# Optimization experiments

Hardware: AMD Instinct MI355X
Metric: run time of the kernel (lower is better)

The kernel has to match this reference:

```python
import jax, jax.numpy as jnp
import numpy as np

IN_C, OUT_C, K = 256, 256, 3

def setup_inputs() -> dict:
    key = jax.random.key(0)
    kx, kw, kb = jax.random.split(key, 3)
    x = jax.random.normal(kx, (32, IN_C, 56, 56), dtype=jnp.float32)
    # kaiming-like scale for conv weight
    fan_in = IN_C * K * K
    weight = jax.random.normal(kw, (OUT_C, IN_C, K, K), dtype=jnp.float32) / np.sqrt(fan_in)
    bias = jax.random.normal(kb, (OUT_C,), dtype=jnp.float32) * 0.01
    return {"x": x, "weight": weight, "bias": bias}

def reference(x, weight, bias):
    # SparseConv2d computes an (approximately lossless, threshold=1e-6)
    # block-sparse conv2d; exact math == dense conv2d, stride 1, pad 1.
    y = jax.lax.conv_general_dilated(
        x, weight,
        window_strides=(1, 1),
        padding=((1, 1), (1, 1)),
        dimension_numbers=("NCHW", "OIHW", "NCHW"),
    )
    return y + bias[None, :, None, None]
```

## Files before the change

kernel.cpp:

```cpp
#include <hip/hip_runtime.h>
#include <hip/hip_bf16.h>

#define IN_C  256
#define OUT_C 256
#define HH 56
#define WW 56
#define NN 32
#define XT_H 58
#define XT_W 64
#define WT_BYTES (8*9*256*32*2)

#define XS_BYTES 24576
#define LDS_TOTAL (2*XS_BYTES)

using short8 = __attribute__((ext_vector_type(8))) short;
using f32x4  = __attribute__((ext_vector_type(4))) float;

__device__ __forceinline__ void gload_lds16(const void* g, void* l) {
  __builtin_amdgcn_global_load_lds((const __attribute__((address_space(1))) void*)g,
                                   (__attribute__((address_space(3))) void*)l,
                                   16, 0, 0);
}

#define VMWAIT(N) asm volatile("s_waitcnt vmcnt(" #N ")" ::: "memory")

__global__ void k_prep(const float* __restrict__ x, const float* __restrict__ w,
                       __hip_bfloat16* __restrict__ wt, __hip_bfloat16* __restrict__ xt) {
  const int b = blockIdx.x, tid = threadIdx.x;

  if (b >= NN * XT_H) {
    const int base = (b - NN * XT_H) * 1024;
#pragma unroll
    for (int k = 0; k < 4; ++k) {
      int idx = base + k * 256 + tid;
      int kw = idx % 3; int t1 = idx / 3;
      int kh = t1 % 3;  int t2 = t1 / 3;
      int ic = t2 % IN_C; int oc = t2 / IN_C;
      int tap = kh * 3 + kw;
      wt[((((ic >> 5) * 9 + tap) * 256 + oc) * 32) + (ic & 31)] = __float2bfloat16(w[idx]);
    }
    return;
  }

  const int n = b / XT_H, hp = b % XT_H;
  __hip_bfloat16* row = xt + (size_t)(n * XT_H + hp) * XT_W * 256;

  if (hp == 0 || hp == XT_H - 1) {
    int4 z; z.x = z.y = z.z = z.w = 0;
#pragma unroll
    for (int k = 0; k < 8; ++k) ((int4*)row)[k * 256 + tid] = z;
    return;
  }

  const int h = hp - 1;
  __shared__ __hip_bfloat16 tile[56][264];

  {
    const int ic = tid;
    const float* src = x + (((size_t)n * IN_C + ic) * HH + h) * WW;
#pragma unroll
    for (int j = 0; j < 14; ++j) {
      float4 v = ((const float4*)src)[j];
      tile[4 * j + 0][ic] = __float2bfloat16(v.x);
      tile[4 * j + 1][ic] = __float2bfloat16(v.y);
      tile[4 * j + 2][ic] = __float2bfloat16(v.z);
      tile[4 * j + 3][ic] = __float2bfloat16(v.w);
    }
  }
  {
    int4 z; z.x = z.y = z.z = z.w = 0;
    int cell = tid >> 5, s = tid & 31;
    int wp = (cell == 0) ? 0 : (56 + cell);
    ((int4*)(row + (size_t)wp * 256))[s] = z;
  }
  __syncthreads();
#pragma unroll
  for (int k = 0; k < 7; ++k) {
    int e = k * 256 + tid;
    int wq = e >> 5, seg = e & 31;
    short8 v = *(const short8*)&tile[wq][seg * 8];
    *(short8*)(row + (size_t)(wq + 1) * 256 + seg * 8) = v;
  }
}

__global__ __launch_bounds__(256, 3) void k_conv(
    const __hip_bfloat16* __restrict__ wt, const __hip_bfloat16* __restrict__ xt,
    const float* __restrict__ bias, float* __restrict__ out) {
  extern __shared__ __align__(16) char lds[];
  char* xs_c = lds;

  const int tid  = threadIdx.x;
  const int wid  = tid >> 6, lane = tid & 63;
  const int cc   = lane & 15, g = lane >> 4;
  const int wn   = wid & 1,  wm = wid >> 1;

  const int work = (blockIdx.x & 7) * 224 + (blockIdx.x >> 3);
  const int n   = work / 56;
  const int rem = work - n * 56;
  const int q   = rem >> 2, oh = rem & 3;
  const int h0  = q * 4;

  int xoff[7];
#pragma unroll
  for (int pt = 0; pt < 7; ++pt) {
    int p = wm * 112 + pt * 16 + cc;
    int rp = p / 56, wp = p - rp * 56;
    xoff[pt] = rp * 4096 + wp * 64 + g * 16;
  }
  const int ocb = oh * 64 + wn * 32;
  const __hip_bfloat16* wlane = wt + (size_t)(ocb + cc) * 32 + g * 8;

  f32x4 acc[2][7];
#pragma unroll
  for (int a = 0; a < 2; ++a)
#pragma unroll
    for (int bb = 0; bb < 7; ++bb) acc[a][bb] = (f32x4){0.f, 0.f, 0.f, 0.f};

  const __hip_bfloat16* xtn = xt + (size_t)(n * XT_H + h0) * XT_W * 256;

  auto stage_x = [&](int buf, int ch) {
#pragma unroll
    for (int i = 0; i < 6; ++i) {
      int s = wid * 6 + i;
      int rowc = s >> 2, colq = s & 3;
      const __hip_bfloat16* src = xtn + (size_t)(rowc * 64 + colq * 16 + (lane >> 2)) * 256
                                      + ch * 32 + (lane & 3) * 8;
      gload_lds16(src, xs_c + buf * XS_BYTES + rowc * 4096 + colq * 1024);
    }
  };
  auto loadw1 = [&](int ph, int oct) -> short8 {
    return *(const short8*)(wlane + (size_t)ph * 8192 + oct * 512);
  };

  short8 wA, wB, wC;

  stage_x(0, 0);
  __builtin_amdgcn_sched_barrier(0);
  wA = loadw1(0, 0);
  wB = loadw1(0, 1);

#define MFMA7(W_, oct_) do {                                                          \
    __builtin_amdgcn_s_setprio(1);                                                    \
    _Pragma("unroll")                                                                 \
    for (int pt = 0; pt < 7; ++pt)                                                    \
      acc[oct_][pt] = __builtin_amdgcn_mfma_f32_16x16x32_bf16(W_, xf[pt], acc[oct_][pt], 0, 0, 0); \
    __builtin_amdgcn_s_setprio(0);                                                    \
  } while (0)

#define PHASE(ph_, kh_, kw_, T0_, T1_, T2_) do {                                      \
    short8 xf[7];                                                                     \
    _Pragma("unroll")                                                                 \
    for (int pt = 0; pt < 7; ++pt)                                                    \
      xf[pt] = *(const short8*)(xb + xoff[pt] + (kh_) * 4096 + (kw_) * 64);           \
    T2_ = loadw1((ph_) + 1, 0);                                                       \
    MFMA7(T0_, 0);                                                                    \
    T0_ = loadw1((ph_) + 1, 1);                                                       \
    MFMA7(T1_, 1);                                                                    \
  } while (0)

  for (int ch = 0; ch < 8; ++ch) {
    VMWAIT(2);
    __builtin_amdgcn_s_barrier();
    if (ch < 7) {
      stage_x((ch + 1) & 1, ch + 1);
      __builtin_amdgcn_sched_barrier(0);
    }
    const char* xb = xs_c + ((ch & 1) ? XS_BYTES : 0);
    const int ph0 = ch * 9;
    PHASE(ph0 + 0, 0, 0, wA, wB, wC);
    PHASE(ph0 + 1, 0, 1, wC, wA, wB);
    PHASE(ph0 + 2, 0, 2, wB, wC, wA);
    PHASE(ph0 + 3, 1, 0, wA, wB, wC);
    PHASE(ph0 + 4, 1, 1, wC, wA, wB);
    PHASE(ph0 + 5, 1, 2, wB, wC, wA);
    PHASE(ph0 + 6, 2, 0, wA, wB, wC);
    PHASE(ph0 + 7, 2, 1, wC, wA, wB);
    PHASE(ph0 + 8, 2, 2, wB, wC, wA);
  }
#undef PHASE
#undef MFMA7

  int rp_[7], wp_[7];
#pragma unroll
  for (int pt = 0; pt < 7; ++pt) {
    int p = wm * 112 + pt * 16 + cc;
    rp_[pt] = p / 56; wp_[pt] = p - rp_[pt] * 56;
  }
#pragma unroll
  for (int oct = 0; oct < 2; ++oct) {
    const int oc0 = ocb + oct * 16 + 4 * g;
#pragma unroll
    for (int r = 0; r < 4; ++r) {
      const float bv = bias[oc0 + r];
      const size_t obase = ((size_t)n * OUT_C + (oc0 + r)) * (HH * WW);
#pragma unroll
      for (int pt = 0; pt < 7; ++pt)
        out[obase + (size_t)(h0 + rp_[pt]) * 56 + wp_[pt]] = acc[oct][pt][r] + bv;
    }
  }
}

extern "C" void kernel_launch(void* const* d_in, const int* in_sizes, int n_in,
                              void* d_out, int out_size, void* d_ws, size_t ws_size,
                              hipStream_t stream) {
  const float* x    = (const float*)d_in[0];
  const float* w    = (const float*)d_in[1];
  const float* bias = (const float*)d_in[2];
  float* out        = (float*)d_out;

  __hip_bfloat16* wt = (__hip_bfloat16*)d_ws;
  __hip_bfloat16* xt = (__hip_bfloat16*)((char*)d_ws + WT_BYTES);

  hipFuncSetAttribute((const void*)k_conv,
                      hipFuncAttributeMaxDynamicSharedMemorySize, LDS_TOTAL);

  k_prep<<<NN * XT_H + 576, 256, 0, stream>>>(x, w, wt, xt);
  k_conv<<<NN * 14 * 4, 256, LDS_TOTAL, stream>>>(wt, xt, bias, out);
}
```

Baseline: 141.4 us.

## Reuse kw=0 LDS fragments via DPP lane shifts for kw=1,2 taps

Instead of reloading input fragments from LDS for each of the three horizontal taps, the kernel loads the kw=0 fragments once per kernel row plus one extra fragment, then builds the kw=1 and kw=2 operands with DPP row-shift and rotate operations across lanes. Boundary lanes are patched with select logic for row wraparound and padding. This cuts LDS read traffic by about two thirds. In exchange it adds VALU DPP instructions and register pressure, and the lane-fixup logic is intricate and could be wrong.

Result: slower. 259.7 us (+83.7%).

```diff
diff --git a/kernel.cpp b/kernel.cpp
--- a/kernel.cpp
+++ b/kernel.cpp
@@ -14,6 +14,7 @@
 #define LDS_TOTAL (2*XS_BYTES)
 
 using short8 = __attribute__((ext_vector_type(8))) short;
+using u32x4  = __attribute__((ext_vector_type(4))) unsigned int;
 using f32x4  = __attribute__((ext_vector_type(4))) float;
 
 __device__ __forceinline__ void gload_lds16(const void* g, void* l) {
@@ -23,6 +24,23 @@
 }
 
 #define VMWAIT(N) asm volatile("s_waitcnt vmcnt(" #N ")" ::: "memory")
+
+template<int CTRL>
+__device__ __forceinline__ u32x4 dpp_rot(u32x4 v) {
+  u32x4 r;
+#pragma unroll
+  for (int i = 0; i < 4; ++i)
+    r[i] = (unsigned)__builtin_amdgcn_update_dpp((int)v[i], (int)v[i], CTRL, 0xF, 0xF, false);
+  return r;
+}
+template<int CTRL>
+__device__ __forceinline__ u32x4 dpp_shl(u32x4 old, u32x4 src) {
+  u32x4 r;
+#pragma unroll
+  for (int i = 0; i < 4; ++i)
+    r[i] = (unsigned)__builtin_amdgcn_update_dpp((int)old[i], (int)src[i], CTRL, 0xF, 0xF, false);
+  return r;
+}
 
 __global__ void k_prep(const float* __restrict__ x, const float* __restrict__ w,
                        __hip_bfloat16* __restrict__ wt, __hip_bfloat16* __restrict__ xt) {
@@ -107,6 +125,8 @@
     int rp = p / 56, wp = p - rp * 56;
     xoff[pt] = rp * 4096 + wp * 64 + g * 16;
   }
+  const int fxoff = (wm * 2 + (cc >= 8 ? 1 : 0)) * 4096 + 56 * 64 + g * 16;
+
   const int ocb = oh * 64 + wn * 32;
   const __hip_bfloat16* wlane = wt + (size_t)(ocb + cc) * 32 + g * 8;
 
@@ -133,29 +153,61 @@
   };
 
   short8 wA, wB, wC;
+  u32x4 X0u[7], XS[7], fxu;
 
   stage_x(0, 0);
   __builtin_amdgcn_sched_barrier(0);
   wA = loadw1(0, 0);
   wB = loadw1(0, 1);
 
-#define MFMA7(W_, oct_) do {                                                          \
+#define MFMA7(XA_, W_, oct_) do {                                                     \
     __builtin_amdgcn_s_setprio(1);                                                    \
     _Pragma("unroll")                                                                 \
     for (int pt = 0; pt < 7; ++pt)                                                    \
-      acc[oct_][pt] = __builtin_amdgcn_mfma_f32_16x16x32_bf16(W_, xf[pt], acc[oct_][pt], 0, 0, 0); \
+      acc[oct_][pt] = __builtin_amdgcn_mfma_f32_16x16x32_bf16(                        \
+          W_, __builtin_bit_cast(short8, XA_[pt]), acc[oct_][pt], 0, 0, 0);           \
     __builtin_amdgcn_s_setprio(0);                                                    \
   } while (0)
 
-#define PHASE(ph_, kh_, kw_, T0_, T1_, T2_) do {                                      \
-    short8 xf[7];                                                                     \
+#define MF2(XA_, ph_, T0_, T1_, T2_) do {                                             \
+    T2_ = loadw1((ph_) + 1, 0);                                                       \
+    MFMA7(XA_, T0_, 0);                                                               \
+    T0_ = loadw1((ph_) + 1, 1);                                                       \
+    MFMA7(XA_, T1_, 1);                                                               \
+  } while (0)
+
+#define PHASE_R(ph_, kh_, T0_, T1_, T2_) do {                                         \
     _Pragma("unroll")                                                                 \
     for (int pt = 0; pt < 7; ++pt)                                                    \
-      xf[pt] = *(const short8*)(xb + xoff[pt] + (kh_) * 4096 + (kw_) * 64);           \
-    T2_ = loadw1((ph_) + 1, 0);                                                       \
-    MFMA7(T0_, 0);                                                                    \
-    T0_ = loadw1((ph_) + 1, 1);                                                       \
-    MFMA7(T1_, 1);                                                                    \
+      X0u[pt] = *(const u32x4*)(xb + xoff[pt] + (kh_) * 4096);                        \
+    fxu = *(const u32x4*)(xb + fxoff + (kh_) * 4096);                                 \
+    MF2(X0u, ph_, T0_, T1_, T2_);                                                     \
+  } while (0)
+
+#define PHASE_1(ph_, T0_, T1_, T2_) do {                                              \
+    _Pragma("unroll")                                                                 \
+    for (int pt = 0; pt < 6; ++pt)                                                    \
+      XS[pt] = dpp_shl<0x101>(dpp_rot<0x12F>(X0u[pt + 1]), X0u[pt]);                  \
+    XS[6] = dpp_shl<0x101>(fxu, X0u[6]);                                              \
+    _Pragma("unroll")                                                                 \
+    for (int i = 0; i < 4; ++i) XS[3][i] = (cc == 7) ? fxu[i] : XS[3][i];             \
+    MF2(XS, ph_, T0_, T1_, T2_);                                                      \
+  } while (0)
+
+#define PHASE_2(ph_, T0_, T1_, T2_) do {                                              \
+    _Pragma("unroll")                                                                 \
+    for (int pt = 0; pt < 6; ++pt)                                                    \
+      XS[pt] = dpp_shl<0x102>(dpp_rot<0x12E>(X0u[pt + 1]), X0u[pt]);                  \
+    {                                                                                 \
+      u32x4 o6;                                                                       \
+      _Pragma("unroll")                                                               \
+      for (int i = 0; i < 4; ++i) o6[i] = (cc == 15) ? 0u : fxu[i];                   \
+      XS[6] = dpp_shl<0x102>(o6, X0u[6]);                                             \
+    }                                                                                 \
+    _Pragma("unroll")                                                                 \
+    for (int i = 0; i < 4; ++i)                                                       \
+      XS[3][i] = (cc == 6) ? fxu[i] : ((cc == 7) ? 0u : XS[3][i]);                    \
+    MF2(XS, ph_, T0_, T1_, T2_);                                                      \
   } while (0)
 
   for (int ch = 0; ch < 8; ++ch) {
@@ -167,17 +219,20 @@
     }
     const char* xb = xs_c + ((ch & 1) ? XS_BYTES : 0);
     const int ph0 = ch * 9;
-    PHASE(ph0 + 0, 0, 0, wA, wB, wC);
-    PHASE(ph0 + 1, 0, 1, wC, wA, wB);
-    PHASE(ph0 + 2, 0, 2, wB, wC, wA);
-    PHASE(ph0 + 3, 1, 0, wA, wB, wC);
-    PHASE(ph0 + 4, 1, 1, wC, wA, wB);
-    PHASE(ph0 + 5, 1, 2, wB, wC, wA);
-    PHASE(ph0 + 6, 2, 0, wA, wB, wC);
-    PHASE(ph0 + 7, 2, 1, wC, wA, wB);
-    PHASE(ph0 + 8, 2, 2, wB, wC, wA);
-  }
-#undef PHASE
+    PHASE_R(ph0 + 0, 0, wA, wB, wC);
+    PHASE_1(ph0 + 1,    wC, wA, wB);
+    PHASE_2(ph0 + 2,    wB, wC, wA);
+    PHASE_R(ph0 + 3, 1, wA, wB, wC);
+    PHASE_1(ph0 + 4,    wC, wA, wB);
+    PHASE_2(ph0 + 5,    wB, wC, wA);
+    PHASE_R(ph0 + 6, 2, wA, wB, wC);
+    PHASE_1(ph0 + 7,    wC, wA, wB);
+    PHASE_2(ph0 + 8,    wB, wC, wA);
+  }
+#undef PHASE_R
+#undef PHASE_1
+#undef PHASE_2
+#undef MF2
 #undef MFMA7
 
   int rp_[7], wp_[7];
```
